# Kernel tuning notes

Measured on AMD Instinct MI355X. Metric: run time of the kernel, lower is better.

Reference implementation:

```python
import jax, jax.numpy as jnp
import numpy as np

N_NODES = 100000
N_EDGES = 1600000
D_IN, D_HID, D_OUT = 128, 128, 64


def _mean_agg(h_src_feat, src, dst, num_nodes):
    # gather source features along edges, scatter-sum into destinations,
    # divide by in-degree (clamped to 1, matching DGL zero-degree handling)
    summed = jax.ops.segment_sum(h_src_feat[src], dst, num_segments=num_nodes)
    deg = jax.ops.segment_sum(jnp.ones((src.shape[0],), h_src_feat.dtype), dst,
                              num_segments=num_nodes)
    return summed / jnp.maximum(deg, 1.0)[:, None]


def setup_inputs() -> dict:
    key = jax.random.key(0)
    ks = jax.random.split(key, 8)
    x = jax.random.normal(ks[0], (N_NODES, D_IN), dtype=jnp.float32)
    src = jax.random.randint(ks[1], (N_EDGES,), 0, N_NODES, dtype=jnp.int64)
    dst = jax.random.randint(ks[2], (N_EDGES,), 0, N_NODES, dtype=jnp.int64)
    s1 = 1.0 / np.sqrt(D_IN)
    s2 = 1.0 / np.sqrt(D_HID)
    W_self1 = jax.random.normal(ks[3], (D_IN, D_HID), dtype=jnp.float32) * s1
    W_neigh1 = jax.random.normal(ks[4], (D_IN, D_HID), dtype=jnp.float32) * s1
    b1 = jnp.zeros((D_HID,), dtype=jnp.float32)
    W_self2 = jax.random.normal(ks[5], (D_HID, D_OUT), dtype=jnp.float32) * s2
    W_neigh2 = jax.random.normal(ks[6], (D_HID, D_OUT), dtype=jnp.float32) * s2
    b2 = jnp.zeros((D_OUT,), dtype=jnp.float32)
    return {"x": x, "src": src, "dst": dst,
            "W_self1": W_self1, "W_neigh1": W_neigh1, "b1": b1,
            "W_self2": W_self2, "W_neigh2": W_neigh2, "b2": b2}


def reference(x, src, dst, W_self1, W_neigh1, b1, W_self2, W_neigh2, b2):
    n = x.shape[0]
    # layer 1: SAGEConv(mean) + ReLU (dropout is identity in eval mode)
    agg1 = _mean_agg(x, src, dst, n)
    h = x @ W_self1 + agg1 @ W_neigh1 + b1
    h = jax.nn.relu(h)
    # layer 2: SAGEConv(mean)
    agg2 = _mean_agg(h, src, dst, n)
    out = h @ W_self2 + agg2 @ W_neigh2 + b2
    return out
```

## Files before the change

### kernel.cpp

```cpp
#include <hip/hip_runtime.h>

#define N_NODES 100000
#define N_EDGES 1600000
#define D 128
#define D_OUT 64
#define MAXDEG 64

#define NBUCK 782
#define BSHIFT 7
#define BCAP  3072
#define NBLK_SPLIT 1000
#define CHUNK 1600
#define NBLK_PACK 25
#define GEMM_BLOCKS 1563

typedef __attribute__((ext_vector_type(8))) short short8;
typedef __attribute__((ext_vector_type(4))) float floatx4;
typedef __attribute__((ext_vector_type(2))) float floatx2;
typedef __attribute__((ext_vector_type(4))) unsigned uint32x4;

__device__ inline unsigned short f2bf(float f) {
    unsigned u = __builtin_bit_cast(unsigned, f);
    u = (u + 0x7fffu + ((u >> 16) & 1u)) >> 16;
    return (unsigned short)u;
}
__device__ inline float bf2f(unsigned u16) {
    return __builtin_bit_cast(float, u16 << 16);
}
__device__ inline unsigned cvt_pk_bf16(float lo, float hi) {
    unsigned r;
    asm("v_cvt_pk_bf16_f32 %0, %1, %2" : "=v"(r) : "v"(lo), "v"(hi));
    return r;
}

template<bool KPERM>
__device__ inline void pack_ncat(const float* __restrict__ Wa, const float* __restrict__ Wb,
                                 int ncA, int ncB, unsigned short* __restrict__ out, int t) {
    int nnt = (ncA + ncB) >> 4;
    int lane = t & 63;
    int nt = (t >> 6) % nnt;
    int kt = t / (64 * nnt);
    int col = nt * 16 + (lane & 15);
    int k0 = kt * 32 + ((lane >> 4) << 3);
    const float* W = (col < ncA) ? Wa : Wb;
    int nc = (col < ncA) ? ncA : ncB;
    int c  = (col < ncA) ? col : col - ncA;
    unsigned short* dstp = out + (size_t)((kt * nnt + nt) * 64 + lane) * 8;
    #pragma unroll
    for (int j = 0; j < 8; ++j) {
        int k = k0 + j;
        int kr = KPERM ? (((k & 7) << 4) | (k >> 3)) : k;
        dstp[j] = f2bf(W[(size_t)kr * nc + c]);
    }
}

__global__ __launch_bounds__(256) void split_pack(
        const int* __restrict__ src, const int* __restrict__ dst,
        int* __restrict__ gcur, int* __restrict__ bucketbuf,
        const float* __restrict__ Ws1, const float* __restrict__ Wn1,
        const float* __restrict__ Ws2, const float* __restrict__ Wn2,
        unsigned short* __restrict__ Wp1, unsigned short* __restrict__ Wp2,
        unsigned char* __restrict__ y8, unsigned char* __restrict__ z8) {
    __shared__ int cnt[NBUCK];
    __shared__ int base_s[NBUCK];
    __shared__ int dstc[CHUNK];
    const int tid = threadIdx.x;
    const int b = blockIdx.x;
    if (b < NBLK_SPLIT) {
        const int e0 = b * CHUNK;
        for (int i = tid; i < NBUCK; i += 256) cnt[i] = 0;
        __syncthreads();
        for (int i = tid; i < CHUNK; i += 256) {
            int d = __builtin_nontemporal_load(dst + e0 + i);
            dstc[i] = d;
            atomicAdd(&cnt[d >> BSHIFT], 1);
        }
        __syncthreads();
        for (int i = tid; i < NBUCK; i += 256) {
            int c = cnt[i];
            base_s[i] = c ? atomicAdd(&gcur[i], c) : 0;
            cnt[i] = 0;
        }
        __syncthreads();
        for (int i = tid; i < CHUNK; i += 256) {
            int d = dstc[i];
            int s = __builtin_nontemporal_load(src + e0 + i);
            int bk = d >> BSHIFT;
            int p = base_s[bk] + atomicAdd(&cnt[bk], 1);
            if (p < BCAP)
                bucketbuf[bk * BCAP + p] = ((d & 127) << 17) | s;
        }
    } else {
        int sub = b - NBLK_SPLIT;
        if (sub < 16)      pack_ncat<false>(Ws1, Wn1, D, D, Wp1, sub * 256 + tid);
        else if (sub < 24) pack_ncat<true >(Ws2, Wn2, D_OUT, D_OUT, Wp2, (sub - 16) * 256 + tid);
        else {
            if (tid < 32)       ((unsigned*)(y8 + (size_t)N_NODES * 128))[tid] = 0;
            else if (tid < 48)  ((unsigned*)(z8 + (size_t)N_NODES * 64))[tid - 32] = 0;
        }
    }
}

template<int NTA, int NTB, bool AF32, int ILV>
__device__ inline void gemm_body(int bid,
        const void* __restrict__ A, const unsigned short* __restrict__ Wp,
        const float* __restrict__ bias, void* __restrict__ OutA,
        unsigned char* __restrict__ OutB, int tid)
{
    const int NT = NTA + NTB;
    const int wave = tid >> 6;
    const int lane = tid & 63;
    const int q = lane >> 4, m = lane & 15;

    int row = bid * 64 + wave * 16 + m;
    int rowc = (row < N_NODES) ? row : (N_NODES - 1);

    floatx4 acc[NT];
    #pragma unroll
    for (int nt = 0; nt < NT; ++nt) acc[nt] = (floatx4){0.f, 0.f, 0.f, 0.f};

    #pragma unroll
    for (int kt = 0; kt < 4; ++kt) {
        short8 af;
        if (AF32) {
            const float* xr = (const float*)A + (size_t)rowc * D + kt * 32 + q * 8;
            float4 f0 = *(const float4*)xr;
            float4 f1 = *(const float4*)(xr + 4);
            uint32x4 t;
            t[0] = cvt_pk_bf16(f0.x, f0.y);
            t[1] = cvt_pk_bf16(f0.z, f0.w);
            t[2] = cvt_pk_bf16(f1.x, f1.y);
            t[3] = cvt_pk_bf16(f1.z, f1.w);
            af = __builtin_bit_cast(short8, t);
        } else {
            af = *(const short8*)((const unsigned short*)A +
                                  (size_t)rowc * D + kt * 32 + q * 8);
        }
        #pragma unroll
        for (int nt = 0; nt < NT; ++nt) {
            short8 bf = *(const short8*)(Wp + (size_t)((kt * NT + nt) * 64 + lane) * 8);
            acc[nt] = __builtin_amdgcn_mfma_f32_16x16x32_bf16(af, bf, acc[nt], 0, 0, 0);
        }
    }

    const int orow_base = bid * 64 + wave * 16 + q * 4;
    if (ILV == 1) {
        float bv[8];
        #pragma unroll
        for (int nt = 0; nt < 8; ++nt) bv[nt] = bias[nt * 16 + m];
        #pragma unroll
        for (int i = 0; i < 4; ++i) {
            int orow = orow_base + i;
            if (orow < N_NODES) {
                uint32x4 pv;
                #pragma unroll
                for (int t = 0; t < 4; ++t)
                    pv[t] = cvt_pk_bf16(acc[2 * t][i]     + bv[2 * t],
                                        acc[2 * t + 1][i] + bv[2 * t + 1]);
                *(uint32x4*)((unsigned short*)OutA + (size_t)orow * 128 + m * 8) = pv;
                int pk0 = __builtin_amdgcn_cvt_pk_fp8_f32(acc[8][i],  acc[9][i],  0,   false);
                pk0     = __builtin_amdgcn_cvt_pk_fp8_f32(acc[10][i], acc[11][i], pk0, true);
                int pk1 = __builtin_amdgcn_cvt_pk_fp8_f32(acc[12][i], acc[13][i], 0,   false);
                pk1     = __builtin_amdgcn_cvt_pk_fp8_f32(acc[14][i], acc[15][i], pk1, true);
                uint2 v8; v8.x = (unsigned)pk0; v8.y = (unsigned)pk1;
                *(uint2*)(OutB + (size_t)orow * 128 + m * 8) = v8;
            }
        }
    } else {
        float bv[4];
        #pragma unroll
        for (int nt = 0; nt < 4; ++nt) bv[nt] = bias[nt * 16 + m];
        #pragma unroll
        for (int i = 0; i < 4; ++i) {
            int orow = orow_base + i;
            if (orow < N_NODES) {
                float4 o;
                o.x = acc[0][i] + bv[0]; o.y = acc[1][i] + bv[1];
                o.z = acc[2][i] + bv[2]; o.w = acc[3][i] + bv[3];
                *(float4*)((float*)OutA + (size_t)orow * 64 + m * 4) = o;
                int pk = __builtin_amdgcn_cvt_pk_fp8_f32(acc[4][i], acc[5][i], 0,  false);
                pk     = __builtin_amdgcn_cvt_pk_fp8_f32(acc[6][i], acc[7][i], pk, true);
                *(unsigned*)(OutB + (size_t)orow * 64 + m * 4) = (unsigned)pk;
            }
        }
    }
}

__global__ __launch_bounds__(256) void gemm1_csr(
        const float* __restrict__ x, const unsigned short* __restrict__ Wp1,
        const float* __restrict__ b1, unsigned short* __restrict__ xs,
        unsigned char* __restrict__ y8,
        const int* __restrict__ gcur, const int* __restrict__ bucketbuf,
        int* __restrict__ dcount, int* __restrict__ csrp)
{
    __shared__ int lcnt[128];
    const int tid = threadIdx.x;
    if (blockIdx.x < NBUCK) {
        const int b = blockIdx.x;
        if (tid < 128) lcnt[tid] = 0;
        __syncthreads();
        int m = gcur[b]; if (m > BCAP) m = BCAP;
        const int* __restrict__ buf = bucketbuf + b * BCAP;
        for (int i = tid; i < m; i += 256) {
            int v = buf[i];
            int dloc = (v >> 17) & 127, s = v & 0x1FFFF;
            int node = (b << BSHIFT) + dloc;
            int slot = atomicAdd(&lcnt[dloc], 1);
            if (slot < MAXDEG && node < N_NODES)
                csrp[((size_t)node << 6) + slot] = s;
        }
        __syncthreads();
        if (tid < 128) {
            int node = (b << BSHIFT) + tid;
            if (node < N_NODES) {
                int c = lcnt[tid]; if (c > MAXDEG) c = MAXDEG;
                dcount[node] = c;
                int cf = (c + 15) & ~15; if (cf > MAXDEG) cf = MAXDEG;
                int* row = csrp + ((size_t)node << 6);
                for (int k = c; k < cf; ++k) row[k] = N_NODES;
            }
        }
    } else {
        gemm_body<8, 8, true, 1>(blockIdx.x - NBUCK, x, Wp1, b1, xs, y8, tid);
    }
}

__global__ __launch_bounds__(256) void gemm2(
        const unsigned short* __restrict__ h, const unsigned short* __restrict__ Wp2,
        const float* __restrict__ b2, float* __restrict__ tmp,
        unsigned char* __restrict__ z8)
{
    gemm_body<4, 4, false, 2>(blockIdx.x, h, Wp2, b2, tmp, z8, threadIdx.x);
}

template<bool L1>
__global__ __launch_bounds__(256) void agg_add(
        const unsigned char* __restrict__ feat, const int* __restrict__ csrp,
        const int* __restrict__ dcount, const void* __restrict__ self,
        void* __restrict__ out)
{
    const int LPE = L1 ? 32 : 16;
    const int EPG = 64 / LPE;
    const int FSH = L1 ? 7 : 6;
    const int NC  = L1 ? 128 : 64;

    int w = (blockIdx.x * 256 + threadIdx.x) >> 6;
    int lane = threadIdx.x & 63;
    if (w >= N_NODES) return;
    int dg = __builtin_amdgcn_readfirstlane(dcount[w]);
    int cf = (dg + 15) & ~15;
    const int g = lane / LPE;
    const int l = lane % LPE;
    int idxv = 0;
    if (lane < cf) idxv = csrp[((size_t)w << 6) + lane];

    floatx2 ac0 = (floatx2){0.f, 0.f};
    floatx2 ac1 = (floatx2){0.f, 0.f};
    for (int j = 0; j < dg; j += 16) {
        #pragma unroll
        for (int u = 0; u < 16 / EPG; ++u) {
            int s = __shfl(idxv, j + u * EPG + g);
            unsigned v = *(const unsigned*)(feat + ((size_t)s << FSH) + (l << 2));
            ac0 += __builtin_amdgcn_cvt_pk_f32_fp8(v, false);
            ac1 += __builtin_amdgcn_cvt_pk_f32_fp8(v, true);
        }
    }
    #pragma unroll
    for (int delta = 32; delta >= LPE; delta >>= 1) {
        ac0.x += __shfl_down(ac0.x, delta); ac0.y += __shfl_down(ac0.y, delta);
        ac1.x += __shfl_down(ac1.x, delta); ac1.y += __shfl_down(ac1.y, delta);
    }
    if (g == 0) {
        float invd = (dg > 0) ? 1.0f / (float)dg : 1.0f;
        if (L1) {
            uint2 sv = *(const uint2*)((const unsigned short*)self + (size_t)w * NC + l * 4);
            float h0 = bf2f(sv.x & 0xffffu)  + ac0.x * invd;
            float h1 = bf2f(sv.x >> 16)      + ac0.y * invd;
            float h2 = bf2f(sv.y & 0xffffu)  + ac1.x * invd;
            float h3 = bf2f(sv.y >> 16)      + ac1.y * invd;
            h0 = fmaxf(h0, 0.f); h1 = fmaxf(h1, 0.f);
            h2 = fmaxf(h2, 0.f); h3 = fmaxf(h3, 0.f);
            uint2 pv;
            pv.x = cvt_pk_bf16(h0, h1);
            pv.y = cvt_pk_bf16(h2, h3);
            *(uint2*)((unsigned short*)out + (size_t)w * NC + l * 4) = pv;
        } else {
            const float* sp = (const float*)self + (size_t)w * NC + l * 4;
            float4 s0 = *(const float4*)sp;
            float v0 = s0.x + ac0.x * invd;
            float v1 = s0.y + ac0.y * invd;
            float v2 = s0.z + ac1.x * invd;
            float v3 = s0.w + ac1.y * invd;
            float* op = (float*)out + (size_t)w * NC;
            op[l]      = v0;
            op[16 + l] = v1;
            op[32 + l] = v2;
            op[48 + l] = v3;
        }
    }
}

extern "C" void kernel_launch(void* const* d_in, const int* in_sizes, int n_in,
                              void* d_out, int out_size, void* d_ws, size_t ws_size,
                              hipStream_t stream) {
    const float* x   = (const float*)d_in[0];
    const int*   src = (const int*)d_in[1];
    const int*   dst = (const int*)d_in[2];
    const float* Ws1 = (const float*)d_in[3];
    const float* Wn1 = (const float*)d_in[4];
    const float* b1  = (const float*)d_in[5];
    const float* Ws2 = (const float*)d_in[6];
    const float* Wn2 = (const float*)d_in[7];
    const float* b2  = (const float*)d_in[8];
    float* out = (float*)d_out;

    const size_t nd = (size_t)N_NODES * D;
    unsigned short* h   = (unsigned short*)d_ws;
    unsigned short* xs  = h + nd;
    float*          tmp = (float*)xs;
    unsigned char*  y8  = (unsigned char*)(xs + nd);
    unsigned char*  z8  = y8 + (size_t)(N_NODES + 1) * D;
    int* dcount = (int*)(z8 + (size_t)(N_NODES + 1) * D_OUT);
    int* csrp   = dcount + N_NODES;
    int* gcur   = csrp + (size_t)N_NODES * MAXDEG;
    int* bucketbuf = gcur + 1024;
    unsigned short* Wp1 = (unsigned short*)(bucketbuf + (size_t)NBUCK * BCAP);
    unsigned short* Wp2 = Wp1 + 32768;

    hipMemsetAsync(gcur, 0, NBUCK * sizeof(int), stream);

    split_pack<<<NBLK_SPLIT + NBLK_PACK, 256, 0, stream>>>(
        src, dst, gcur, bucketbuf, Ws1, Wn1, Ws2, Wn2, Wp1, Wp2, y8, z8);

    const int agg_blocks = (N_NODES * 64 + 255) / 256;

    gemm1_csr<<<NBUCK + GEMM_BLOCKS, 256, 0, stream>>>(
        x, Wp1, b1, xs, y8, gcur, bucketbuf, dcount, csrp);
    agg_add<true ><<<agg_blocks, 256, 0, stream>>>(y8, csrp, dcount, xs, h);
    gemm2<<<GEMM_BLOCKS, 256, 0, stream>>>(h, Wp2, b2, tmp, z8);
    agg_add<false><<<agg_blocks, 256, 0, stream>>>(z8, csrp, dcount, tmp, out);
}
```

Baseline: 284.5 us.

## Replace global-atomic edge bucketing with per-block slack regions and separate CSR build

Edge splitting now writes each block's edges into a fixed-size slot region per (bucket, block), with no global atomic counters and no memset. The split is fused with the first GEMM launch, and a separate kernel compacts the regions into padded CSR rows. Aggregation now fills unused lanes with the zero-row index instead of writing padding into the CSR. The aim is to remove global atomic contention and the memset launch. In exchange it adds a serial per-thread compaction pass with scattered reads, takes CSR building out of overlap with the GEMM, and silently drops edges if a region overflows its 24 slots.

```diff
diff --git a/kernel.cpp b/kernel.cpp
--- a/kernel.cpp
+++ b/kernel.cpp
@@ -8,10 +8,10 @@
 
 #define NBUCK 782
 #define BSHIFT 7
-#define BCAP  3072
-#define NBLK_SPLIT 1000
-#define CHUNK 1600
-#define NBLK_PACK 25
+#define BMASK 127
+#define NSPL 500
+#define CHUNK 3200
+#define SLACK 24
 #define GEMM_BLOCKS 1563
 
 typedef __attribute__((ext_vector_type(8))) short short8;
@@ -54,50 +54,17 @@
     }
 }
 
-__global__ __launch_bounds__(256) void split_pack(
-        const int* __restrict__ src, const int* __restrict__ dst,
-        int* __restrict__ gcur, int* __restrict__ bucketbuf,
+__global__ __launch_bounds__(256) void pack_zero(
         const float* __restrict__ Ws1, const float* __restrict__ Wn1,
         const float* __restrict__ Ws2, const float* __restrict__ Wn2,
         unsigned short* __restrict__ Wp1, unsigned short* __restrict__ Wp2,
         unsigned char* __restrict__ y8, unsigned char* __restrict__ z8) {
-    __shared__ int cnt[NBUCK];
-    __shared__ int base_s[NBUCK];
-    __shared__ int dstc[CHUNK];
-    const int tid = threadIdx.x;
-    const int b = blockIdx.x;
-    if (b < NBLK_SPLIT) {
-        const int e0 = b * CHUNK;
-        for (int i = tid; i < NBUCK; i += 256) cnt[i] = 0;
-        __syncthreads();
-        for (int i = tid; i < CHUNK; i += 256) {
-            int d = __builtin_nontemporal_load(dst + e0 + i);
-            dstc[i] = d;
-            atomicAdd(&cnt[d >> BSHIFT], 1);
-        }
-        __syncthreads();
-        for (int i = tid; i < NBUCK; i += 256) {
-            int c = cnt[i];
-            base_s[i] = c ? atomicAdd(&gcur[i], c) : 0;
-            cnt[i] = 0;
-        }
-        __syncthreads();
-        for (int i = tid; i < CHUNK; i += 256) {
-            int d = dstc[i];
-            int s = __builtin_nontemporal_load(src + e0 + i);
-            int bk = d >> BSHIFT;
-            int p = base_s[bk] + atomicAdd(&cnt[bk], 1);
-            if (p < BCAP)
-                bucketbuf[bk * BCAP + p] = ((d & 127) << 17) | s;
-        }
-    } else {
-        int sub = b - NBLK_SPLIT;
-        if (sub < 16)      pack_ncat<false>(Ws1, Wn1, D, D, Wp1, sub * 256 + tid);
-        else if (sub < 24) pack_ncat<true >(Ws2, Wn2, D_OUT, D_OUT, Wp2, (sub - 16) * 256 + tid);
-        else {
-            if (tid < 32)       ((unsigned*)(y8 + (size_t)N_NODES * 128))[tid] = 0;
-            else if (tid < 48)  ((unsigned*)(z8 + (size_t)N_NODES * 64))[tid - 32] = 0;
-        }
+    const int tid = threadIdx.x, b = blockIdx.x;
+    if (b < 16)      pack_ncat<false>(Ws1, Wn1, D, D, Wp1, b * 256 + tid);
+    else if (b < 24) pack_ncat<true >(Ws2, Wn2, D_OUT, D_OUT, Wp2, (b - 16) * 256 + tid);
+    else {
+        if (tid < 32)       ((unsigned*)(y8 + (size_t)N_NODES * 128))[tid] = 0;
+        else if (tid < 48)  ((unsigned*)(z8 + (size_t)N_NODES * 64))[tid - 32] = 0;
     }
 }
 
@@ -186,42 +153,68 @@
     }
 }
 
-__global__ __launch_bounds__(256) void gemm1_csr(
+__global__ __launch_bounds__(256) void split_gemm1(
+        const int* __restrict__ src, const int* __restrict__ dst,
+        int* __restrict__ cnt, int* __restrict__ bucketbuf,
         const float* __restrict__ x, const unsigned short* __restrict__ Wp1,
         const float* __restrict__ b1, unsigned short* __restrict__ xs,
-        unsigned char* __restrict__ y8,
-        const int* __restrict__ gcur, const int* __restrict__ bucketbuf,
+        unsigned char* __restrict__ y8)
+{
+    const int tid = threadIdx.x;
+    if (blockIdx.x < NSPL) {
+        __shared__ int lcnt[NBUCK];
+        const int b = blockIdx.x;
+        const int e0 = b * CHUNK;
+        for (int i = tid; i < NBUCK; i += 256) lcnt[i] = 0;
+        __syncthreads();
+        for (int i = tid; i < CHUNK; i += 256) {
+            int d = __builtin_nontemporal_load(dst + e0 + i);
+            int s = __builtin_nontemporal_load(src + e0 + i);
+            int bk = d >> BSHIFT;
+            int p = atomicAdd(&lcnt[bk], 1);
+            if (p < SLACK)
+                bucketbuf[(size_t)(bk * NSPL + b) * SLACK + p] = ((d & BMASK) << 17) | s;
+        }
+        __syncthreads();
+        for (int i = tid; i < NBUCK; i += 256) {
+            int c = lcnt[i];
+            cnt[i * NSPL + b] = (c > SLACK) ? SLACK : c;
+        }
+    } else {
+        gemm_body<8, 8, true, 1>(blockIdx.x - NSPL, x, Wp1, b1, xs, y8, tid);
+    }
+}
+
+__global__ __launch_bounds__(256) void csr_build(
+        const int* __restrict__ cnt, const int* __restrict__ bucketbuf,
         int* __restrict__ dcount, int* __restrict__ csrp)
 {
     __shared__ int lcnt[128];
-    const int tid = threadIdx.x;
-    if (blockIdx.x < NBUCK) {
-        const int b = blockIdx.x;
-        if (tid < 128) lcnt[tid] = 0;
-        __syncthreads();
-        int m = gcur[b]; if (m > BCAP) m = BCAP;
-        const int* __restrict__ buf = bucketbuf + b * BCAP;
-        for (int i = tid; i < m; i += 256) {
-            int v = buf[i];
-            int dloc = (v >> 17) & 127, s = v & 0x1FFFF;
+    __shared__ int cnt_s[NSPL];
+    const int tid = threadIdx.x, b = blockIdx.x;
+    for (int i = tid; i < NSPL; i += 256) cnt_s[i] = cnt[b * NSPL + i];
+    if (tid < 128) lcnt[tid] = 0;
+    __syncthreads();
+    const int* __restrict__ reg = bucketbuf + (size_t)b * NSPL * SLACK;
+    for (int sg = tid; sg < NSPL; sg += 256) {
+        int c = cnt_s[sg];
+        const int* __restrict__ p = reg + sg * SLACK;
+        for (int j = 0; j < c; ++j) {
+            int v = p[j];
+            int dloc = (v >> 17) & BMASK, s = v & 0x1FFFF;
             int node = (b << BSHIFT) + dloc;
             int slot = atomicAdd(&lcnt[dloc], 1);
             if (slot < MAXDEG && node < N_NODES)
                 csrp[((size_t)node << 6) + slot] = s;
         }
-        __syncthreads();
-        if (tid < 128) {
-            int node = (b << BSHIFT) + tid;
-            if (node < N_NODES) {
-                int c = lcnt[tid]; if (c > MAXDEG) c = MAXDEG;
-                dcount[node] = c;
-                int cf = (c + 15) & ~15; if (cf > MAXDEG) cf = MAXDEG;
-                int* row = csrp + ((size_t)node << 6);
-                for (int k = c; k < cf; ++k) row[k] = N_NODES;
-            }
-        }
-    } else {
-        gemm_body<8, 8, true, 1>(blockIdx.x - NBUCK, x, Wp1, b1, xs, y8, tid);
+    }
+    __syncthreads();
+    if (tid < 128) {
+        int node = (b << BSHIFT) + tid;
+        if (node < N_NODES) {
+            int c = lcnt[tid];
+            dcount[node] = (c > MAXDEG) ? MAXDEG : c;
+        }
     }
 }
 
@@ -248,11 +241,10 @@
     int lane = threadIdx.x & 63;
     if (w >= N_NODES) return;
     int dg = __builtin_amdgcn_readfirstlane(dcount[w]);
-    int cf = (dg + 15) & ~15;
     const int g = lane / LPE;
     const int l = lane % LPE;
-    int idxv = 0;
-    if (lane < cf) idxv = csrp[((size_t)w << 6) + lane];
+    int idxv = N_NODES;
+    if (lane < dg) idxv = csrp[((size_t)w << 6) + lane];
 
     floatx2 ac0 = (floatx2){0.f, 0.f};
     floatx2 ac1 = (floatx2){0.f, 0.f};
@@ -322,20 +314,17 @@
     unsigned char*  z8  = y8 + (size_t)(N_NODES + 1) * D;
     int* dcount = (int*)(z8 + (size_t)(N_NODES + 1) * D_OUT);
     int* csrp   = dcount + N_NODES;
-    int* gcur   = csrp + (size_t)N_NODES * MAXDEG;
-    int* bucketbuf = gcur + 1024;
-    unsigned short* Wp1 = (unsigned short*)(bucketbuf + (size_t)NBUCK * BCAP);
+    int* cnt    = csrp + (size_t)N_NODES * MAXDEG;
+    int* bucketbuf = cnt + NBUCK * NSPL;
+    unsigned short* Wp1 = (unsigned short*)(bucketbuf + (size_t)NBUCK * NSPL * SLACK);
     unsigned short* Wp2 = Wp1 + 32768;
 
-    hipMemsetAsync(gcur, 0, NBUCK * sizeof(int), stream);
-
-    split_pack<<<NBLK_SPLIT + NBLK_PACK, 256, 0, stream>>>(
-        src, dst, gcur, bucketbuf, Ws1, Wn1, Ws2, Wn2, Wp1, Wp2, y8, z8);
-
     const int agg_blocks = (N_NODES * 64 + 255) / 256;
 
-    gemm1_csr<<<NBUCK + GEMM_BLOCKS, 256, 0, stream>>>(
-        x, Wp1, b1, xs, y8, gcur, bucketbuf, dcount, csrp);
+    pack_zero<<<25, 256, 0, stream>>>(Ws1, Wn1, Ws2, Wn2, Wp1, Wp2, y8, z8);
+    split_gemm1<<<NSPL + GEMM_BLOCKS, 256, 0, stream>>>(
+        src, dst, cnt, bucketbuf, x, Wp1, b1, xs, y8);
+    csr_build<<<NBUCK, 256, 0, stream>>>(cnt, bucketbuf, dcount, csrp);
     agg_add<true ><<<agg_blocks, 256, 0, stream>>>(y8, csrp, dcount, xs, h);
     gemm2<<<GEMM_BLOCKS, 256, 0, stream>>>(h, Wp2, b2, tmp, z8);
     agg_add<false><<<agg_blocks, 256, 0, stream>>>(z8, csrp, dcount, tmp, out);
```

Result: slower. 292.4 us (+2.8%).
